# Optimization experiments

Measured on AMD Instinct MI355X. Metric: run time of the kernel, lower is better.

The kernel has to match this reference:

```python
import jax, jax.numpy as jnp
import numpy as np

N_NODES = 50000
N_EDGES = 800000
D_MODEL = 128
N_HEAD = 8
D_HEAD = D_MODEL // N_HEAD  # 16
D_FF = 2 * D_MODEL
EPS = 1e-5


def _layer_norm(x, g=None, b=None):
    mu = jnp.mean(x, axis=-1, keepdims=True)
    var = jnp.mean((x - mu) ** 2, axis=-1, keepdims=True)
    y = (x - mu) * jax.lax.rsqrt(var + EPS)
    if g is not None:
        y = y * g + b
    return y


def setup_inputs() -> dict:
    key = jax.random.key(0)
    ks = jax.random.split(key, 14)
    w = lambda k, shp: jax.random.normal(k, shp, dtype=jnp.float32) * 0.05
    return {
        "bond_embedding": jax.random.normal(ks[0], (N_EDGES, D_MODEL), dtype=jnp.float32),
        "node_embedding": jax.random.normal(ks[1], (N_NODES, D_MODEL), dtype=jnp.float32),
        "basic_attn": jax.random.uniform(ks[2], (N_EDGES, 1), dtype=jnp.float32),
        "Wk": w(ks[3], (D_MODEL, D_MODEL)),
        "Wq": w(ks[4], (D_MODEL, D_MODEL)),
        "Wv": w(ks[5], (D_MODEL, D_MODEL)),
        "W_dis": w(ks[6], (N_HEAD, 1)),
        "W_beta": w(ks[7], (1, 3 * D_MODEL)),
        "W1": w(ks[8], (D_FF, D_MODEL)),
        "W2": w(ks[9], (D_MODEL, D_FF)),
        "ln1_g": jnp.ones((D_MODEL,), dtype=jnp.float32),
        "ln1_b": jnp.zeros((D_MODEL,), dtype=jnp.float32),
        "src": jax.random.randint(ks[10], (N_EDGES,), 0, N_NODES, dtype=jnp.int32),
        "dst": jax.random.randint(ks[11], (N_EDGES,), 0, N_NODES, dtype=jnp.int32),
    }


def reference(bond_embedding, node_embedding, basic_attn, Wk, Wq, Wv, W_dis,
              W_beta, W1, W2, ln1_g, ln1_b, src, dst):
    # projections -> per-head layout
    v = (bond_embedding @ Wv.T).reshape(N_EDGES, N_HEAD, D_HEAD)  # edge values
    k = (node_embedding @ Wk.T).reshape(N_NODES, N_HEAD, D_HEAD)
    q = (node_embedding @ Wq.T).reshape(N_NODES, N_HEAD, D_HEAD)

    # u_dot_v('k','q'): per-edge per-head dot product, scaled by sqrt(d_head)
    att = jnp.einsum("ehd,ehd->eh", k[src], q[dst]) / jnp.sqrt(jnp.float32(D_HEAD))
    # distance-decay bias: Linear(1 -> num_head) on per-edge scalar
    logits = att + basic_attn @ W_dis.T  # [E, H]

    # edge_softmax over incoming edges of each dst node (per head)
    m = jax.ops.segment_max(logits, dst, num_segments=N_NODES)
    m = jnp.where(jnp.isfinite(m), m, 0.0)  # isolated nodes
    p = jnp.exp(logits - m[dst])
    s = jax.ops.segment_sum(p, dst, num_segments=N_NODES)
    a = p / s[dst]  # [E, H]

    # weighted scatter-sum of edge values to dst nodes
    ft = jax.ops.segment_sum(v * a[..., None], dst, num_segments=N_NODES)
    he = ft.reshape(N_NODES, D_MODEL)

    # beta gating
    beta = jax.nn.sigmoid(
        jnp.concatenate([he, node_embedding, he - node_embedding], axis=-1) @ W_beta.T
    )  # [N, 1]
    he = beta * node_embedding + (1.0 - beta) * he

    # PoswiseFeedForwardNet: LN -> FFN -> residual -> fresh (non-affine) LN
    residual = he
    h = _layer_norm(he, ln1_g, ln1_b)
    h = jax.nn.relu(h @ W1.T) @ W2.T
    return _layer_norm(h + residual)
```

## Files before the change

### kernel.cpp

```cpp
#include <hip/hip_runtime.h>
#include <hip/hip_bf16.h>

#define N_NODES 50000
#define N_EDGES 800000
#define D 128
#define NH 8
#define DH 16
#define DFF 256
#define LN_EPS 1e-5f
#define GN 16
#define NPB 32
#define SCAN_BS 512
#define NSCAN ((N_NODES + SCAN_BS - 1) / SCAN_BS)

typedef __attribute__((ext_vector_type(8))) short bf16x8;
typedef __attribute__((ext_vector_type(8))) unsigned short u16x8;
typedef __attribute__((ext_vector_type(4))) float f32x4;
typedef unsigned short ushort_t;

__device__ __forceinline__ float wred(float v) {
#pragma unroll
    for (int o = 32; o; o >>= 1) v += __shfl_xor(v, o);
    return v;
}

__device__ __forceinline__ short f2b(float f) {
    unsigned u = __float_as_uint(f);
    unsigned r = u + 0x7fffu + ((u >> 16) & 1u);
    return (short)(r >> 16);
}
__device__ __forceinline__ float b2f(unsigned short u) {
    return __uint_as_float((unsigned)u << 16);
}

__global__ __launch_bounds__(256) void k_zero(int* __restrict__ p) {
    int i = blockIdx.x * 256 + threadIdx.x;
    if (i < N_NODES) p[i] = 0;
}

__global__ __launch_bounds__(128) void k_qkproj(
    const float* __restrict__ x, const float* __restrict__ Wk,
    const float* __restrict__ Wq, ushort_t* __restrict__ kout,
    ushort_t* __restrict__ qout) {
    __shared__ float xs[16][128];
    const int t = threadIdx.x;
    const int nb = blockIdx.x * 16;
#pragma unroll
    for (int r = 0; r < 16; ++r) xs[r][t] = x[(size_t)(nb + r) * D + t];
    __syncthreads();
    const float4* wk4 = (const float4*)(Wk + (size_t)t * D);
    const float4* wq4 = (const float4*)(Wq + (size_t)t * D);
    float ka[16] = {}, qa[16] = {};
#pragma unroll 4
    for (int i4 = 0; i4 < 32; ++i4) {
        float4 wk = wk4[i4], wq = wq4[i4];
#pragma unroll
        for (int r = 0; r < 16; ++r) {
            float4 xv = *(const float4*)&xs[r][i4 * 4];
            ka[r] += wk.x * xv.x + wk.y * xv.y + wk.z * xv.z + wk.w * xv.w;
            qa[r] += wq.x * xv.x + wq.y * xv.y + wq.z * xv.z + wq.w * xv.w;
        }
    }
#pragma unroll
    for (int r = 0; r < 16; ++r) {
        kout[(size_t)(nb + r) * D + t] = (ushort_t)f2b(ka[r]);
        qout[(size_t)(nb + r) * D + t] = (ushort_t)f2b(qa[r]);
    }
}

__global__ __launch_bounds__(256) void k_hist(const int* __restrict__ dst,
                                              int* __restrict__ deg) {
    int e = blockIdx.x * 256 + threadIdx.x;
    atomicAdd(&deg[dst[e]], 1);
}

__global__ __launch_bounds__(SCAN_BS) void k_scan1(
    const int* __restrict__ deg, int* __restrict__ scanout,
    int* __restrict__ bsum) {
    __shared__ int ss[SCAN_BS];
    const int t = threadIdx.x;
    const int i = blockIdx.x * SCAN_BS + t;
    int v = (i < N_NODES) ? deg[i] : 0;
    ss[t] = v;
    __syncthreads();
    for (int off = 1; off < SCAN_BS; off <<= 1) {
        int a = (t >= off) ? ss[t - off] : 0;
        __syncthreads();
        ss[t] += a;
        __syncthreads();
    }
    if (i < N_NODES) scanout[i] = ss[t] - v;
    if (t == SCAN_BS - 1) bsum[blockIdx.x] = ss[t];
}

__global__ __launch_bounds__(128) void k_scan2(int* __restrict__ bsum) {
    __shared__ int ss[128];
    const int t = threadIdx.x;
    int v = (t < NSCAN) ? bsum[t] : 0;
    ss[t] = v;
    __syncthreads();
    for (int off = 1; off < 128; off <<= 1) {
        int a = (t >= off) ? ss[t - off] : 0;
        __syncthreads();
        ss[t] += a;
        __syncthreads();
    }
    if (t < NSCAN) bsum[t] = ss[t] - v;
}

__global__ __launch_bounds__(256) void k_scan3(
    const int* __restrict__ scanout, const int* __restrict__ bsum,
    int* __restrict__ rowstart, int* __restrict__ cursor) {
    int i = blockIdx.x * 256 + threadIdx.x;
    if (i < N_NODES) {
        int rs = scanout[i] + bsum[i / SCAN_BS];
        rowstart[i] = rs;
        cursor[i] = rs;
    }
    if (i == 0) rowstart[N_NODES] = N_EDGES;
}

__global__ __launch_bounds__(256) void k_fill(const int* __restrict__ dst,
                                              int* __restrict__ cursor,
                                              int* __restrict__ eidx) {
    int e = blockIdx.x * 256 + threadIdx.x;
    int pos = atomicAdd(&cursor[dst[e]], 1);
    eidx[pos] = e;
}

__global__ __launch_bounds__(256) void k_attn(
    const ushort_t* __restrict__ kv, const ushort_t* __restrict__ qv,
    const float* __restrict__ basic, const float* __restrict__ Wdis,
    const int* __restrict__ src, const int* __restrict__ rowstart,
    const int* __restrict__ eidx, float* __restrict__ aperm,
    float* __restrict__ sinv) {
    const int t = threadIdx.x;
    const int lane = t & 63, wv = t >> 6;
    const int n = blockIdx.x * 4 + wv;
    const int j = lane >> 3, h = lane & 7;
    const int rs = rowstart[n], re = rowstart[n + 1];
    const float wd = Wdis[h];
    const ushort_t* qp = qv + (size_t)n * D + h * DH;
    u16x8 q0 = *(const u16x8*)qp;
    u16x8 q1 = *(const u16x8*)(qp + 8);
    float qf[16];
#pragma unroll
    for (int i = 0; i < 8; ++i) { qf[i] = b2f(q0[i]); qf[8 + i] = b2f(q1[i]); }

    float sl = 0.f;
    for (int base = rs; base < re; base += 8) {
        int pos = base + j;
        if (pos < re) {
            int e = eidx[pos];
            int sc = src[e];
            const ushort_t* kp = kv + (size_t)sc * D + h * DH;
            u16x8 k0 = *(const u16x8*)kp;
            u16x8 k1 = *(const u16x8*)(kp + 8);
            float acc = 0.f;
#pragma unroll
            for (int i = 0; i < 8; ++i) acc += qf[i] * b2f(k0[i]);
#pragma unroll
            for (int i = 0; i < 8; ++i) acc += qf[8 + i] * b2f(k1[i]);
            float p = expf(acc * 0.25f + basic[e] * wd);
            aperm[(size_t)pos * NH + h] = p;
            sl += p;
        }
    }
    sl += __shfl_xor(sl, 8);
    sl += __shfl_xor(sl, 16);
    sl += __shfl_xor(sl, 32);
    if (lane < 8) sinv[(size_t)n * NH + h] = (sl > 0.f) ? 1.f / sl : 0.f;
}

__global__ __launch_bounds__(256) void k_hsum(
    const float* __restrict__ bond, const float* __restrict__ Wv,
    const float* __restrict__ aperm, const float* __restrict__ sinv,
    const int* __restrict__ rowstart, const int* __restrict__ eidx,
    float* __restrict__ ft) {
    __shared__ short slds[8 * 16 * 128];
    __shared__ float sivlds[GN * 8];
    __shared__ int srs[GN + 1];
    const int t = threadIdx.x;
    const int lane = t & 63, w = t >> 6;
    const int lr = lane & 15, lg = lane >> 4;
    const int n0 = blockIdx.x * GN;
    if (t < GN + 1) srs[t] = rowstart[n0 + t];
    if (t < GN * 8) sivlds[t] = sinv[(size_t)n0 * 8 + t];
    __syncthreads();

    const int c0 = lane * 2;
    const int chunk = lane >> 2;
    const int elo = (lane * 2) & 7;

#pragma unroll
    for (int i = 0; i < 4; ++i) {
        int ln = w + i * 4;
        int rs = srs[ln], re = srs[ln + 1];
        float sacc[8][2];
#pragma unroll
        for (int h = 0; h < 8; ++h) { sacc[h][0] = 0.f; sacc[h][1] = 0.f; }
        int pos = rs;
        for (; pos + 2 <= re; pos += 2) {
            int e0 = eidx[pos], e1 = eidx[pos + 1];
            float2 b0 = *(const float2*)&bond[(size_t)e0 * D + c0];
            float2 b1 = *(const float2*)&bond[(size_t)e1 * D + c0];
            float4 a00 = *(const float4*)&aperm[(size_t)pos * 8];
            float4 a01 = *(const float4*)&aperm[(size_t)pos * 8 + 4];
            float4 a10 = *(const float4*)&aperm[(size_t)(pos + 1) * 8];
            float4 a11 = *(const float4*)&aperm[(size_t)(pos + 1) * 8 + 4];
            const float a0v[8] = {a00.x, a00.y, a00.z, a00.w,
                                  a01.x, a01.y, a01.z, a01.w};
            const float a1v[8] = {a10.x, a10.y, a10.z, a10.w,
                                  a11.x, a11.y, a11.z, a11.w};
#pragma unroll
            for (int h = 0; h < 8; ++h) {
                sacc[h][0] += a0v[h] * b0.x + a1v[h] * b1.x;
                sacc[h][1] += a0v[h] * b0.y + a1v[h] * b1.y;
            }
        }
        for (; pos < re; ++pos) {
            int e = eidx[pos];
            float2 b = *(const float2*)&bond[(size_t)e * D + c0];
            float4 a0 = *(const float4*)&aperm[(size_t)pos * 8];
            float4 a1 = *(const float4*)&aperm[(size_t)pos * 8 + 4];
            const float av[8] = {a0.x, a0.y, a0.z, a0.w,
                                 a1.x, a1.y, a1.z, a1.w};
#pragma unroll
            for (int h = 0; h < 8; ++h) {
                sacc[h][0] += av[h] * b.x;
                sacc[h][1] += av[h] * b.y;
            }
        }
#pragma unroll
        for (int h = 0; h < 8; ++h) {
            float siv = sivlds[ln * 8 + h];
            unsigned u = (unsigned)(unsigned short)f2b(sacc[h][0] * siv) |
                         ((unsigned)(unsigned short)f2b(sacc[h][1] * siv) << 16);
            *(unsigned*)&slds[(h * 16 + ln) * 128 +
                              ((chunk ^ (ln & 7)) << 3) + elo] = u;
        }
    }
    __syncthreads();

    bf16x8 bfr[2][4];
#pragma unroll
    for (int nn = 0; nn < 2; ++nn) {
        int col = (2 * w + nn) * 16 + lr;
#pragma unroll
        for (int ks = 0; ks < 4; ++ks) {
            const float4* gp = (const float4*)(Wv + (size_t)col * D + ks * 32 + lg * 8);
            float4 f0 = gp[0], f1 = gp[1];
            bf16x8 v;
            v[0] = f2b(f0.x); v[1] = f2b(f0.y); v[2] = f2b(f0.z); v[3] = f2b(f0.w);
            v[4] = f2b(f1.x); v[5] = f2b(f1.y); v[6] = f2b(f1.z); v[7] = f2b(f1.w);
            bfr[nn][ks] = v;
        }
    }
    f32x4 acc[2];
#pragma unroll
    for (int nn = 0; nn < 2; ++nn) acc[nn] = (f32x4){0.f, 0.f, 0.f, 0.f};
#pragma unroll
    for (int ks = 0; ks < 4; ++ks) {
        int ck = ks * 4 + lg;
#pragma unroll
        for (int nn = 0; nn < 2; ++nn) {
            int h = 2 * w + nn;
            bf16x8 sf = *(const bf16x8*)&slds[(h * 16 + lr) * 128 +
                                              ((ck ^ (lr & 7)) << 3)];
            acc[nn] = __builtin_amdgcn_mfma_f32_16x16x32_bf16(
                bfr[nn][ks], sf, acc[nn], 0, 0, 0);
        }
    }
#pragma unroll
    for (int nn = 0; nn < 2; ++nn) {
        float4 o = {acc[nn][0], acc[nn][1], acc[nn][2], acc[nn][3]};
        *(float4*)&ft[(size_t)(n0 + lr) * D + (2 * w + nn) * 16 + lg * 4] = o;
    }
}

__global__ __launch_bounds__(256, 2) void k_node(
    const float* __restrict__ ft, const float* __restrict__ x,
    const float* __restrict__ Wb, const float* __restrict__ W1,
    const float* __restrict__ W2, const float* __restrict__ g_ln,
    const float* __restrict__ b_ln, float* __restrict__ out) {
    __shared__ float hs[NPB][132];
    __shared__ short hA[NPB * 128];
    __shared__ short hid[NPB * 256];
    __shared__ float ylds[NPB][132];
    const int t = threadIdx.x;
    const int lane = t & 63, w = t >> 6;
    const int lr = lane & 15, lg = lane >> 4;
    const int n0 = blockIdx.x * NPB;
    const int c0 = lane * 2;

    const float2 wb0 = *(const float2*)&Wb[c0];
    const float2 wb1 = *(const float2*)&Wb[128 + c0];
    const float2 wb2 = *(const float2*)&Wb[256 + c0];
    const float2 gv = *(const float2*)&g_ln[c0];
    const float2 bv = *(const float2*)&b_ln[c0];
#pragma unroll
    for (int i = 0; i < 8; ++i) {
        int n = w * 8 + i;
        int gn = n0 + n;
        float2 fv = {0.f, 0.f}, xv = {0.f, 0.f};
        if (gn < N_NODES) {
            fv = *(const float2*)&ft[(size_t)gn * D + c0];
            xv = *(const float2*)&x[(size_t)gn * D + c0];
        }
        float part = fv.x * wb0.x + fv.y * wb0.y + xv.x * wb1.x + xv.y * wb1.y +
                     (fv.x - xv.x) * wb2.x + (fv.y - xv.y) * wb2.y;
        float beta = 1.f / (1.f + expf(-wred(part)));
        float hex = beta * xv.x + (1.f - beta) * fv.x;
        float hey = beta * xv.y + (1.f - beta) * fv.y;
        hs[n][c0] = hex;
        hs[n][c0 + 1] = hey;
        float mu = wred(hex + hey) * (1.f / 128.f);
        float dx = hex - mu, dy = hey - mu;
        float var = wred(dx * dx + dy * dy) * (1.f / 128.f);
        float rs = rsqrtf(var + LN_EPS);
        float h0 = dx * rs * gv.x + bv.x;
        float h1 = dy * rs * gv.y + bv.y;
        unsigned u = (unsigned)(unsigned short)f2b(h0) |
                     ((unsigned)(unsigned short)f2b(h1) << 16);
        int phys = (lane >> 2) ^ (n & 7);
        ((unsigned*)hA)[n * 64 + phys * 4 + (lane & 3)] = u;
    }
    __syncthreads();

    {
        bf16x8 b1[4][4];
#pragma unroll
        for (int nt = 0; nt < 4; ++nt) {
            int col = w * 64 + nt * 16 + lr;
#pragma unroll
            for (int ks = 0; ks < 4; ++ks) {
                const float4* gp = (const float4*)(W1 + (size_t)col * D + ks * 32 + lg * 8);
                float4 f0 = gp[0], f1 = gp[1];
                bf16x8 v;
                v[0] = f2b(f0.x); v[1] = f2b(f0.y); v[2] = f2b(f0.z); v[3] = f2b(f0.w);
                v[4] = f2b(f1.x); v[5] = f2b(f1.y); v[6] = f2b(f1.z); v[7] = f2b(f1.w);
                b1[nt][ks] = v;
            }
        }
        f32x4 acc1[2][4];
#pragma unroll
        for (int m = 0; m < 2; ++m)
#pragma unroll
            for (int nt = 0; nt < 4; ++nt) acc1[m][nt] = (f32x4){0.f, 0.f, 0.f, 0.f};
#pragma unroll
        for (int ks = 0; ks < 4; ++ks) {
            int chunk = ks * 4 + lg;
#pragma unroll
            for (int m = 0; m < 2; ++m) {
                int row = m * 16 + lr;
                bf16x8 af = *(const bf16x8*)&hA[row * 128 + ((chunk ^ (row & 7)) << 3)];
#pragma unroll
                for (int nt = 0; nt < 4; ++nt)
                    acc1[m][nt] = __builtin_amdgcn_mfma_f32_16x16x32_bf16(
                        af, b1[nt][ks], acc1[m][nt], 0, 0, 0);
            }
        }
#pragma unroll
        for (int m = 0; m < 2; ++m)
#pragma unroll
            for (int nt = 0; nt < 4; ++nt)
#pragma unroll
                for (int r = 0; r < 4; ++r) {
                    int node = m * 16 + lg * 4 + r;
                    int col = w * 64 + nt * 16 + lr;
                    float v = fmaxf(acc1[m][nt][r], 0.f);
                    hid[node * 256 + (((col >> 3) ^ (node & 7)) << 3) + (col & 7)] = f2b(v);
                }
    }
    __syncthreads();

    {
        bf16x8 b2[2][8];
#pragma unroll
        for (int nt = 0; nt < 2; ++nt) {
            int col = w * 32 + nt * 16 + lr;
#pragma unroll
            for (int ks = 0; ks < 8; ++ks) {
                const float4* gp = (const float4*)(W2 + (size_t)col * DFF + ks * 32 + lg * 8);
                float4 f0 = gp[0], f1 = gp[1];
                bf16x8 v;
                v[0] = f2b(f0.x); v[1] = f2b(f0.y); v[2] = f2b(f0.z); v[3] = f2b(f0.w);
                v[4] = f2b(f1.x); v[5] = f2b(f1.y); v[6] = f2b(f1.z); v[7] = f2b(f1.w);
                b2[nt][ks] = v;
            }
        }
        f32x4 acc2[2][2];
#pragma unroll
        for (int m = 0; m < 2; ++m)
#pragma unroll
            for (int nt = 0; nt < 2; ++nt) acc2[m][nt] = (f32x4){0.f, 0.f, 0.f, 0.f};
#pragma unroll
        for (int ks = 0; ks < 8; ++ks) {
            int chunk = ks * 4 + lg;
#pragma unroll
            for (int m = 0; m < 2; ++m) {
                int row = m * 16 + lr;
                bf16x8 af = *(const bf16x8*)&hid[row * 256 + ((chunk ^ (row & 7)) << 3)];
#pragma unroll
                for (int nt = 0; nt < 2; ++nt)
                    acc2[m][nt] = __builtin_amdgcn_mfma_f32_16x16x32_bf16(
                        af, b2[nt][ks], acc2[m][nt], 0, 0, 0);
            }
        }
#pragma unroll
        for (int m = 0; m < 2; ++m)
#pragma unroll
            for (int nt = 0; nt < 2; ++nt)
#pragma unroll
                for (int r = 0; r < 4; ++r) {
                    int node = m * 16 + lg * 4 + r;
                    int col = w * 32 + nt * 16 + lr;
                    ylds[node][col] = acc2[m][nt][r] + hs[node][col];
                }
    }
    __syncthreads();

#pragma unroll
    for (int i = 0; i < 8; ++i) {
        int n = w * 8 + i;
        int gn = n0 + n;
        float y0 = ylds[n][c0], y1 = ylds[n][c0 + 1];
        float mu = wred(y0 + y1) * (1.f / 128.f);
        float d0 = y0 - mu, d1 = y1 - mu;
        float var = wred(d0 * d0 + d1 * d1) * (1.f / 128.f);
        float rs = rsqrtf(var + LN_EPS);
        if (gn < N_NODES) {
            float2 o = {d0 * rs, d1 * rs};
            *(float2*)&out[(size_t)gn * D + c0] = o;
        }
    }
}

extern "C" void kernel_launch(void* const* d_in, const int* in_sizes, int n_in,
                              void* d_out, int out_size, void* d_ws, size_t ws_size,
                              hipStream_t stream) {
    const float* bond = (const float*)d_in[0];
    const float* x    = (const float*)d_in[1];
    const float* basic= (const float*)d_in[2];
    const float* Wk   = (const float*)d_in[3];
    const float* Wq   = (const float*)d_in[4];
    const float* Wv   = (const float*)d_in[5];
    const float* Wdis = (const float*)d_in[6];
    const float* Wb   = (const float*)d_in[7];
    const float* W1   = (const float*)d_in[8];
    const float* W2   = (const float*)d_in[9];
    const float* g_ln = (const float*)d_in[10];
    const float* b_ln = (const float*)d_in[11];
    const int* src    = (const int*)d_in[12];
    const int* dst    = (const int*)d_in[13];
    float* out = (float*)d_out;

    ushort_t* kbf = (ushort_t*)d_ws;
    ushort_t* qbf = kbf + (size_t)N_NODES * D;
    float* aperm = (float*)(qbf + (size_t)N_NODES * D);
    float* ftb   = aperm + (size_t)N_EDGES * NH;
    float* sinvb = ftb + (size_t)N_NODES * D;
    int* deg     = (int*)(sinvb + (size_t)N_NODES * NH);
    int* scanout = deg + N_NODES;
    int* bsum    = scanout + N_NODES;
    int* rowstart= bsum + 128;
    int* cursor  = rowstart + N_NODES + 1;
    int* eidx    = cursor + N_NODES;

    k_zero<<<(N_NODES + 255) / 256, 256, 0, stream>>>(deg);
    k_qkproj<<<N_NODES / 16, 128, 0, stream>>>(x, Wk, Wq, kbf, qbf);
    k_hist<<<N_EDGES / 256, 256, 0, stream>>>(dst, deg);
    k_scan1<<<NSCAN, SCAN_BS, 0, stream>>>(deg, scanout, bsum);
    k_scan2<<<1, 128, 0, stream>>>(bsum);
    k_scan3<<<(N_NODES + 255) / 256, 256, 0, stream>>>(scanout, bsum, rowstart, cursor);
    k_fill<<<N_EDGES / 256, 256, 0, stream>>>(dst, cursor, eidx);
    k_attn<<<N_NODES / 4, 256, 0, stream>>>(kbf, qbf, basic, Wdis, src,
                                            rowstart, eidx, aperm, sinvb);
    k_hsum<<<N_NODES / GN, 256, 0, stream>>>(bond, Wv, aperm, sinvb,
                                             rowstart, eidx, ftb);
    k_node<<<(N_NODES + NPB - 1) / NPB, 256, 0, stream>>>(ftb, x, Wb, W1, W2,
                                                          g_ln, b_ln, out);
}
```

Baseline: 521.8 us.

## Fuse attention logit/softmax computation into the aggregation kernel

Removes the separate k_attn kernel and computes per-edge per-head logits, exponentials and softmax denominators inside k_hsum. Each wave's lanes load pairs of bf16 k values, do a shuffle reduction across 8 lanes per head, and broadcast the per-head weight with shuffles. This drops the round trip of the E×8 aperm buffer and the sinv buffer through global memory, and one launch. In exchange it adds shuffle and exp work to the aggregation loop, plus extra gathers of src and k rows in the inner loop.

```diff
diff --git a/kernel.cpp b/kernel.cpp
--- a/kernel.cpp
+++ b/kernel.cpp
@@ -128,112 +128,93 @@
     eidx[pos] = e;
 }
 
-__global__ __launch_bounds__(256) void k_attn(
-    const ushort_t* __restrict__ kv, const ushort_t* __restrict__ qv,
-    const float* __restrict__ basic, const float* __restrict__ Wdis,
-    const int* __restrict__ src, const int* __restrict__ rowstart,
-    const int* __restrict__ eidx, float* __restrict__ aperm,
-    float* __restrict__ sinv) {
-    const int t = threadIdx.x;
-    const int lane = t & 63, wv = t >> 6;
-    const int n = blockIdx.x * 4 + wv;
-    const int j = lane >> 3, h = lane & 7;
-    const int rs = rowstart[n], re = rowstart[n + 1];
-    const float wd = Wdis[h];
-    const ushort_t* qp = qv + (size_t)n * D + h * DH;
-    u16x8 q0 = *(const u16x8*)qp;
-    u16x8 q1 = *(const u16x8*)(qp + 8);
-    float qf[16];
-#pragma unroll
-    for (int i = 0; i < 8; ++i) { qf[i] = b2f(q0[i]); qf[8 + i] = b2f(q1[i]); }
-
-    float sl = 0.f;
-    for (int base = rs; base < re; base += 8) {
-        int pos = base + j;
-        if (pos < re) {
-            int e = eidx[pos];
-            int sc = src[e];
-            const ushort_t* kp = kv + (size_t)sc * D + h * DH;
-            u16x8 k0 = *(const u16x8*)kp;
-            u16x8 k1 = *(const u16x8*)(kp + 8);
-            float acc = 0.f;
-#pragma unroll
-            for (int i = 0; i < 8; ++i) acc += qf[i] * b2f(k0[i]);
-#pragma unroll
-            for (int i = 0; i < 8; ++i) acc += qf[8 + i] * b2f(k1[i]);
-            float p = expf(acc * 0.25f + basic[e] * wd);
-            aperm[(size_t)pos * NH + h] = p;
-            sl += p;
-        }
-    }
-    sl += __shfl_xor(sl, 8);
-    sl += __shfl_xor(sl, 16);
-    sl += __shfl_xor(sl, 32);
-    if (lane < 8) sinv[(size_t)n * NH + h] = (sl > 0.f) ? 1.f / sl : 0.f;
-}
-
 __global__ __launch_bounds__(256) void k_hsum(
-    const float* __restrict__ bond, const float* __restrict__ Wv,
-    const float* __restrict__ aperm, const float* __restrict__ sinv,
-    const int* __restrict__ rowstart, const int* __restrict__ eidx,
-    float* __restrict__ ft) {
+    const float* __restrict__ bond, const ushort_t* __restrict__ kbf,
+    const ushort_t* __restrict__ qbf, const float* __restrict__ basic,
+    const float* __restrict__ Wdis, const int* __restrict__ src,
+    const float* __restrict__ Wv, const int* __restrict__ rowstart,
+    const int* __restrict__ eidx, float* __restrict__ ft) {
     __shared__ short slds[8 * 16 * 128];
-    __shared__ float sivlds[GN * 8];
     __shared__ int srs[GN + 1];
     const int t = threadIdx.x;
     const int lane = t & 63, w = t >> 6;
     const int lr = lane & 15, lg = lane >> 4;
     const int n0 = blockIdx.x * GN;
     if (t < GN + 1) srs[t] = rowstart[n0 + t];
-    if (t < GN * 8) sivlds[t] = sinv[(size_t)n0 * 8 + t];
     __syncthreads();
 
     const int c0 = lane * 2;
     const int chunk = lane >> 2;
     const int elo = (lane * 2) & 7;
+    const float wd = Wdis[lane >> 3];
 
 #pragma unroll
     for (int i = 0; i < 4; ++i) {
         int ln = w + i * 4;
+        int node = n0 + ln;
         int rs = srs[ln], re = srs[ln + 1];
+        unsigned qu = *(const unsigned*)&qbf[(size_t)node * D + c0];
+        float q0 = b2f((ushort_t)(qu & 0xffffu));
+        float q1 = b2f((ushort_t)(qu >> 16));
         float sacc[8][2];
-#pragma unroll
-        for (int h = 0; h < 8; ++h) { sacc[h][0] = 0.f; sacc[h][1] = 0.f; }
+        float psum[8];
+#pragma unroll
+        for (int h = 0; h < 8; ++h) {
+            sacc[h][0] = 0.f; sacc[h][1] = 0.f; psum[h] = 0.f;
+        }
         int pos = rs;
         for (; pos + 2 <= re; pos += 2) {
             int e0 = eidx[pos], e1 = eidx[pos + 1];
+            int s0 = src[e0], s1 = src[e1];
             float2 b0 = *(const float2*)&bond[(size_t)e0 * D + c0];
             float2 b1 = *(const float2*)&bond[(size_t)e1 * D + c0];
-            float4 a00 = *(const float4*)&aperm[(size_t)pos * 8];
-            float4 a01 = *(const float4*)&aperm[(size_t)pos * 8 + 4];
-            float4 a10 = *(const float4*)&aperm[(size_t)(pos + 1) * 8];
-            float4 a11 = *(const float4*)&aperm[(size_t)(pos + 1) * 8 + 4];
-            const float a0v[8] = {a00.x, a00.y, a00.z, a00.w,
-                                  a01.x, a01.y, a01.z, a01.w};
-            const float a1v[8] = {a10.x, a10.y, a10.z, a10.w,
-                                  a11.x, a11.y, a11.z, a11.w};
+            unsigned k0u = *(const unsigned*)&kbf[(size_t)s0 * D + c0];
+            unsigned k1u = *(const unsigned*)&kbf[(size_t)s1 * D + c0];
+            float ba0 = basic[e0], ba1 = basic[e1];
+            float part0 = q0 * b2f((ushort_t)(k0u & 0xffffu)) +
+                          q1 * b2f((ushort_t)(k0u >> 16));
+            float part1 = q0 * b2f((ushort_t)(k1u & 0xffffu)) +
+                          q1 * b2f((ushort_t)(k1u >> 16));
+            part0 += __shfl_xor(part0, 1);
+            part1 += __shfl_xor(part1, 1);
+            part0 += __shfl_xor(part0, 2);
+            part1 += __shfl_xor(part1, 2);
+            part0 += __shfl_xor(part0, 4);
+            part1 += __shfl_xor(part1, 4);
+            float p0 = expf(part0 * 0.25f + ba0 * wd);
+            float p1 = expf(part1 * 0.25f + ba1 * wd);
 #pragma unroll
             for (int h = 0; h < 8; ++h) {
-                sacc[h][0] += a0v[h] * b0.x + a1v[h] * b1.x;
-                sacc[h][1] += a0v[h] * b0.y + a1v[h] * b1.y;
+                float ph0 = __shfl(p0, h * 8);
+                float ph1 = __shfl(p1, h * 8);
+                psum[h] += ph0 + ph1;
+                sacc[h][0] += ph0 * b0.x + ph1 * b1.x;
+                sacc[h][1] += ph0 * b0.y + ph1 * b1.y;
             }
         }
         for (; pos < re; ++pos) {
             int e = eidx[pos];
+            int sc = src[e];
             float2 b = *(const float2*)&bond[(size_t)e * D + c0];
-            float4 a0 = *(const float4*)&aperm[(size_t)pos * 8];
-            float4 a1 = *(const float4*)&aperm[(size_t)pos * 8 + 4];
-            const float av[8] = {a0.x, a0.y, a0.z, a0.w,
-                                 a1.x, a1.y, a1.z, a1.w};
+            unsigned ku = *(const unsigned*)&kbf[(size_t)sc * D + c0];
+            float ba = basic[e];
+            float part = q0 * b2f((ushort_t)(ku & 0xffffu)) +
+                         q1 * b2f((ushort_t)(ku >> 16));
+            part += __shfl_xor(part, 1);
+            part += __shfl_xor(part, 2);
+            part += __shfl_xor(part, 4);
+            float p = expf(part * 0.25f + ba * wd);
 #pragma unroll
             for (int h = 0; h < 8; ++h) {
-                sacc[h][0] += av[h] * b.x;
-                sacc[h][1] += av[h] * b.y;
+                float ph = __shfl(p, h * 8);
+                psum[h] += ph;
+                sacc[h][0] += ph * b.x;
+                sacc[h][1] += ph * b.y;
             }
         }
 #pragma unroll
         for (int h = 0; h < 8; ++h) {
-            float siv = sivlds[ln * 8 + h];
+            float siv = (psum[h] > 0.f) ? 1.f / psum[h] : 0.f;
             unsigned u = (unsigned)(unsigned short)f2b(sacc[h][0] * siv) |
                          ((unsigned)(unsigned short)f2b(sacc[h][1] * siv) << 16);
             *(unsigned*)&slds[(h * 16 + ln) * 128 +
@@ -457,10 +438,8 @@
 
     ushort_t* kbf = (ushort_t*)d_ws;
     ushort_t* qbf = kbf + (size_t)N_NODES * D;
-    float* aperm = (float*)(qbf + (size_t)N_NODES * D);
-    float* ftb   = aperm + (size_t)N_EDGES * NH;
-    float* sinvb = ftb + (size_t)N_NODES * D;
-    int* deg     = (int*)(sinvb + (size_t)N_NODES * NH);
+    float* ftb   = (float*)(qbf + (size_t)N_NODES * D);
+    int* deg     = (int*)(ftb + (size_t)N_NODES * D);
     int* scanout = deg + N_NODES;
     int* bsum    = scanout + N_NODES;
     int* rowstart= bsum + 128;
@@ -474,10 +453,8 @@
     k_scan2<<<1, 128, 0, stream>>>(bsum);
     k_scan3<<<(N_NODES + 255) / 256, 256, 0, stream>>>(scanout, bsum, rowstart, cursor);
     k_fill<<<N_EDGES / 256, 256, 0, stream>>>(dst, cursor, eidx);
-    k_attn<<<N_NODES / 4, 256, 0, stream>>>(kbf, qbf, basic, Wdis, src,
-                                            rowstart, eidx, aperm, sinvb);
-    k_hsum<<<N_NODES / GN, 256, 0, stream>>>(bond, Wv, aperm, sinvb,
-                                             rowstart, eidx, ftb);
+    k_hsum<<<N_NODES / GN, 256, 0, stream>>>(bond, kbf, qbf, basic, Wdis, src,
+                                             Wv, rowstart, eidx, ftb);
     k_node<<<(N_NODES + NPB - 1) / NPB, 256, 0, stream>>>(ftb, x, Wb, W1, W2,
                                                           g_ln, b_ln, out);
 }
```

Result: slower. 556.9 us (+6.7%).
